# Kernel tuning notes

Measured on AMD Instinct MI355X. Metric: run time of the kernel, lower is better.

The kernel has to match this reference:

```python
import jax, jax.numpy as jnp
import numpy as np
import math

B, C, H, W = 8, 64, 256, 256
E, NH = 256, 8
HD = E // NH  # 32


def get_coords(h, w):
    xx, yy = jnp.meshgrid(jnp.arange(h, dtype=jnp.float32), jnp.arange(w, dtype=jnp.float32), indexing='ij')
    return jnp.stack((xx.reshape(-1), yy.reshape(-1)), axis=-1)  # [N, 2]


def setup_inputs() -> dict:
    key = jax.random.key(0)
    ks = jax.random.split(key, 12)
    def xavier(k, shape):
        fan_out, fan_in = shape
        a = math.sqrt(6.0 / (fan_in + fan_out))
        return jax.random.uniform(k, shape, jnp.float32, -a, a)
    x = jax.random.normal(ks[0], (B, C, H, W), jnp.float32)
    z = jax.random.normal(ks[1], (B, C), jnp.float32)
    pos = jax.random.uniform(ks[2], (B, NH, 2), jnp.float32) * (H - 1)
    Wq = xavier(ks[3], (E, C)); bq = jnp.zeros((E,), jnp.float32)
    Wk = xavier(ks[4], (E, C)); bk = jnp.zeros((E,), jnp.float32)
    Wv = xavier(ks[5], (E, C)); bv = jnp.zeros((E,), jnp.float32)
    Wp = xavier(ks[6], (HD, 2)); bp = jax.random.uniform(ks[7], (HD,), jnp.float32, -1.0, 1.0) / math.sqrt(2.0)
    return {"x": x, "z": z, "pos": pos, "Wq": Wq, "bq": bq, "Wk": Wk, "bk": bk,
            "Wv": Wv, "bv": bv, "Wp": Wp, "bp": bp}


def reference(x, z, pos, Wq, bq, Wk, bk, Wv, bv, Wp, bp):
    b, c, h, w = x.shape
    n = h * w
    x_flat = x.reshape(b, c, n).transpose(0, 2, 1)          # [B, N, C]
    pos_grid = get_coords(h, w)                              # [N, 2]
    q = (z @ Wq.T + bq).reshape(b, NH, HD)                   # [B, H, hd]
    k = (x_flat @ Wk.T + bk).reshape(b, n, NH, HD)           # [B, N, H, hd]
    # relative-position modulation of keys
    rel = pos_grid[None, :, None, :] - pos[:, None, :, :]    # [B, N, H, 2]
    qxk = rel @ Wp.T + bp                                    # [B, N, H, hd]
    k = k * qxk
    v = x_flat @ Wv.T + bv                                   # [B, N, E]
    attn_logits = jnp.einsum('bhc,bnhc->bnh', q, k) / math.sqrt(HD)
    attention = jax.nn.softmax(attn_logits, axis=1)          # softmax over N
    pos_out = jnp.einsum('bnh,nx->bhx', attention, pos_grid) # [B, H, 2]
    values = jnp.einsum('bnh,bnc->bhc', attention, v)        # [B, H, E]
    return (values, pos_out)
```

## Files before the change

### kernel.cpp

```cpp
#include <hip/hip_runtime.h>

#define NN    65536
#define NSUB  128
#define NBLK  (NN/NSUB)

typedef short bf16x8 __attribute__((ext_vector_type(8)));
typedef float f32x4v __attribute__((ext_vector_type(4)));
typedef unsigned short ushort_t;
typedef unsigned int uint_t;

#define XSTR   72
#define XHI_B  0
#define XLO_B  18432
#define LGA_B  18432
#define LGSTR  28
#define RED_B  36864
#define SMEM_BYTES 37056

#define WTHI_B  0
#define WTLO_B  32768
#define CJ_B    65536
#define PM_B    66304
#define PL_B    197376
#define PSP_B   328448
#define PSX_B   590592
#define Q_B     8979200
#define QSTR    68

__device__ __forceinline__ uint_t bf16_rne_bits(float f) {
  uint_t u = __float_as_uint(f);
  return (u + 0x7FFFu + ((u >> 16) & 1u)) >> 16;
}
template <int CTRL>
__device__ __forceinline__ float dpp_add(float x) {
  int t = __builtin_amdgcn_update_dpp(0, __float_as_int(x), CTRL, 0xf, 0xf, false);
  return x + __int_as_float(t);
}
template <int CTRL>
__device__ __forceinline__ float dpp_maxs(float x) {
  int t = __builtin_amdgcn_update_dpp((int)0xFF800000u, __float_as_int(x), CTRL, 0xf, 0xf, false);
  return fmaxf(x, __int_as_float(t));
}
__device__ __forceinline__ float wave_sum(float x) {
  x = dpp_add<0x111>(x); x = dpp_add<0x112>(x); x = dpp_add<0x114>(x);
  x = dpp_add<0x118>(x); x = dpp_add<0x142>(x); x = dpp_add<0x143>(x);
  return __int_as_float(__builtin_amdgcn_readlane(__float_as_int(x), 63));
}
__device__ __forceinline__ float wave_max(float x) {
  x = dpp_maxs<0x111>(x); x = dpp_maxs<0x112>(x); x = dpp_maxs<0x114>(x);
  x = dpp_maxs<0x118>(x); x = dpp_maxs<0x142>(x); x = dpp_maxs<0x143>(x);
  return __int_as_float(__builtin_amdgcn_readlane(__float_as_int(x), 63));
}

__global__ __launch_bounds__(64) void prep_kernel(
    const float* __restrict__ z,  const float* __restrict__ Wq, const float* __restrict__ bq,
    const float* __restrict__ Wk, const float* __restrict__ bk,
    const float* __restrict__ Wp, const float* __restrict__ bp,
    ushort_t* __restrict__ WThi, ushort_t* __restrict__ WTlo, float* __restrict__ Cj)
{
  const int h = blockIdx.x, b = blockIdx.y, t = threadIdx.x;
  __shared__ float q[32];
  if (t < 32) {
    const int e = h*32 + t;
    float a = bq[e];
    const float* zr = z + b*64;
    const float* wr = Wq + e*64;
    #pragma unroll 8
    for (int c = 0; c < 64; ++c) a += zr[c]*wr[c];
    q[t] = a;
  }
  __syncthreads();
  const int c = t;
  float w[3] = {0.f, 0.f, 0.f};
  #pragma unroll 4
  for (int hd = 0; hd < 32; ++hd) {
    const float qk = q[hd] * Wk[(h*32+hd)*64 + c];
    w[0] += qk * bp[hd];
    w[1] += qk * Wp[hd*2+0];
    w[2] += qk * Wp[hd*2+1];
  }
  #pragma unroll
  for (int j = 0; j < 3; ++j) {
    const int coeff = h*3 + j;
    const uint_t hb = bf16_rne_bits(w[j]);
    const float  fh = __uint_as_float(hb << 16);
    const uint_t lb = bf16_rne_bits(w[j] - fh);
    WThi[(b*32 + coeff)*64 + c] = (ushort_t)hb;
    WTlo[(b*32 + coeff)*64 + c] = (ushort_t)lb;
  }
  if (h == 0) {
    #pragma unroll
    for (int r = 0; r < 8; ++r) {
      WThi[(b*32 + 24 + r)*64 + c] = 0;
      WTlo[(b*32 + 24 + r)*64 + c] = 0;
    }
  }
  if (t < 3) {
    float s = 0.f;
    for (int hd = 0; hd < 32; ++hd) {
      const float m = (t == 0) ? bp[hd] : Wp[hd*2 + (t-1)];
      s += q[hd] * m * bk[h*32+hd];
    }
    Cj[b*24 + h*3 + t] = s;
  }
}

__global__ __launch_bounds__(128, 2) void main_kernel(
    const float* __restrict__ x, const float* __restrict__ pos,
    const ushort_t* __restrict__ WThi, const ushort_t* __restrict__ WTlo,
    const float* __restrict__ Cj,
    float* __restrict__ Pm, float* __restrict__ Pl,
    float* __restrict__ Psp, float* __restrict__ Psx)
{
  extern __shared__ char smc[];
  ushort_t* xhi = (ushort_t*)(smc + XHI_B);
  float*    lga = (float*)(smc + LGA_B);
  float*    red = (float*)(smc + RED_B);
  const int t   = threadIdx.x;
  const int blk = blockIdx.x;
  const int b   = blockIdx.y;
  const int n0  = blk * NSUB;
  const int wid = t >> 6, lid = t & 63;
  const int c0  = lid & 15, q4 = lid >> 4;

  bf16x8 bh[2][2], bl[2][2];
  {
    const ushort_t* wtb_h = WThi + b*2048;
    const ushort_t* wtb_l = WTlo + b*2048;
    #pragma unroll
    for (int nt = 0; nt < 2; ++nt)
      #pragma unroll
      for (int ks = 0; ks < 2; ++ks) {
        const int off = (nt*16 + c0)*64 + ks*32 + q4*8;
        bh[nt][ks] = *(const bf16x8*)(wtb_h + off);
        bl[nt][ks] = *(const bf16x8*)(wtb_l + off);
      }
  }

  {
    const float* xg = x + (size_t)b*64*NN + n0 + t;
    #pragma unroll
    for (int half = 0; half < 2; ++half) {
      float v[32];
      #pragma unroll
      for (int i = 0; i < 32; ++i) v[i] = xg[(size_t)(half*32+i)*NN];
      #pragma unroll
      for (int cc2 = 0; cc2 < 2; ++cc2) {
        const int cc = half*2 + cc2;
        uint_t hb[16], lb[16];
        #pragma unroll
        for (int i = 0; i < 16; ++i) {
          const float f = v[cc2*16+i];
          hb[i] = bf16_rne_bits(f);
          lb[i] = bf16_rne_bits(f - __uint_as_float(hb[i] << 16));
        }
        uint4 H0 = make_uint4(hb[0]|(hb[1]<<16), hb[2]|(hb[3]<<16), hb[4]|(hb[5]<<16), hb[6]|(hb[7]<<16));
        uint4 H1 = make_uint4(hb[8]|(hb[9]<<16), hb[10]|(hb[11]<<16), hb[12]|(hb[13]<<16), hb[14]|(hb[15]<<16));
        uint4 L0 = make_uint4(lb[0]|(lb[1]<<16), lb[2]|(lb[3]<<16), lb[4]|(lb[5]<<16), lb[6]|(lb[7]<<16));
        uint4 L1 = make_uint4(lb[8]|(lb[9]<<16), lb[10]|(lb[11]<<16), lb[12]|(lb[13]<<16), lb[14]|(lb[15]<<16));
        char* dh = smc + XHI_B + t*144 + cc*32;
        char* dl = smc + XLO_B + t*144 + cc*32;
        *(uint4*)(dh)      = H0;  *(uint4*)(dh + 16) = H1;
        *(uint4*)(dl)      = L0;  *(uint4*)(dl + 16) = L1;
      }
    }
  }

  float cj[24];
  {
    const float* cjp = Cj + b*24;
    #pragma unroll
    for (int k = 0; k < 24; ++k) cj[k] = cjp[k];
  }
  const int gx = blk >> 1;
  float rxh[8], py[8];
  #pragma unroll
  for (int h = 0; h < 8; ++h) {
    rxh[h] = (float)gx - pos[(b*8+h)*2 + 0];
    py[h]  = pos[(b*8+h)*2 + 1];
  }

  __syncthreads();

  f32x4v acc[4][2];
  #pragma unroll
  for (int mt = 0; mt < 4; ++mt) { acc[mt][0] = (f32x4v)0.f; acc[mt][1] = (f32x4v)0.f; }
  {
    const int mrow0 = wid*64;
    #pragma unroll
    for (int mt = 0; mt < 4; ++mt) {
      const int row = mrow0 + mt*16 + c0;
      const ushort_t* ph = xhi + row*XSTR + q4*8;
      const ushort_t* pl = (ushort_t*)(smc + XLO_B) + row*XSTR + q4*8;
      bf16x8 ah0 = *(const bf16x8*)(ph);
      bf16x8 ah1 = *(const bf16x8*)(ph + 32);
      bf16x8 al0 = *(const bf16x8*)(pl);
      bf16x8 al1 = *(const bf16x8*)(pl + 32);
      #pragma unroll
      for (int nt = 0; nt < 2; ++nt) {
        f32x4v a = acc[mt][nt];
        a = __builtin_amdgcn_mfma_f32_16x16x32_bf16(ah0, bh[nt][0], a, 0, 0, 0);
        a = __builtin_amdgcn_mfma_f32_16x16x32_bf16(ah1, bh[nt][1], a, 0, 0, 0);
        a = __builtin_amdgcn_mfma_f32_16x16x32_bf16(ah0, bl[nt][0], a, 0, 0, 0);
        a = __builtin_amdgcn_mfma_f32_16x16x32_bf16(ah1, bl[nt][1], a, 0, 0, 0);
        a = __builtin_amdgcn_mfma_f32_16x16x32_bf16(al0, bh[nt][0], a, 0, 0, 0);
        a = __builtin_amdgcn_mfma_f32_16x16x32_bf16(al1, bh[nt][1], a, 0, 0, 0);
        acc[mt][nt] = a;
      }
    }
  }
  __syncthreads();

  {
    const int mrow0 = wid*64;
    #pragma unroll
    for (int mt = 0; mt < 4; ++mt)
      #pragma unroll
      for (int r = 0; r < 4; ++r) {
        const int prow = mrow0 + mt*16 + q4*4 + r;
        lga[prow*LGSTR + c0] = acc[mt][0][r];
        if (c0 < 8) lga[prow*LGSTR + 16 + c0] = acc[mt][1][r];
      }
  }
  __syncthreads();

  float a24[24];
  {
    const float4* ap = (const float4*)(lga + t*LGSTR);
    #pragma unroll
    for (int r = 0; r < 6; ++r) *(float4*)(a24 + 4*r) = ap[r];
  }
  const float tf = (float)(((blk & 1) << 7) + t);
  float lg[8];
  #pragma unroll
  for (int h = 0; h < 8; ++h) {
    const float a0 = a24[h*3+0] + cj[h*3+0];
    const float a1 = a24[h*3+1] + cj[h*3+1];
    const float a2 = a24[h*3+2] + cj[h*3+2];
    lg[h] = (a0 + rxh[h]*a1 + (tf - py[h])*a2) * 0.17677669529663687f;
  }

  #pragma unroll
  for (int h = 0; h < 8; ++h) {
    const float m = wave_max(lg[h]);
    if (lid == 0) red[h*2 + wid] = m;
  }
  __syncthreads();

  float p[8];
  #pragma unroll
  for (int h = 0; h < 8; ++h) {
    const float M = fmaxf(red[h*2+0], red[h*2+1]);
    p[h] = __expf(lg[h] - M);
  }
  #pragma unroll
  for (int h = 0; h < 8; ++h) {
    const float sp  = wave_sum(p[h]);
    const float spj = wave_sum(p[h] * tf);
    if (lid == 0) { red[16 + h*2 + wid] = sp; red[32 + h*2 + wid] = spj; }
  }
  __syncthreads();

  if (t < 8) {
    const int base = (b*NBLK + blk)*8 + t;
    const float M  = fmaxf(red[t*2+0], red[t*2+1]);
    const float L  = red[16+t*2+0] + red[16+t*2+1];
    const float SJ = red[32+t*2+0] + red[32+t*2+1];
    Pm[base] = M;
    Pl[base] = L;
    Psp[base*2+0] = (float)gx * L;
    Psp[base*2+1] = SJ;
  }

  float aB[8];
  #pragma unroll
  for (int h = 0; h < 8; ++h) aB[h] = 0.f;
  {
    const ushort_t* xrow = xhi + (wid*64)*XSTR + lid;
    #pragma unroll 8
    for (int j = 0; j < 64; ++j) {
      const float xv = __uint_as_float(((uint_t)xrow[j*XSTR]) << 16);
      #pragma unroll
      for (int h = 0; h < 8; ++h) {
        const float pj = __int_as_float(__builtin_amdgcn_readlane(__float_as_int(p[h]), j));
        aB[h] = fmaf(pj, xv, aB[h]);
      }
    }
  }
  __syncthreads();
  {
    float* pstage = (float*)smc;
    #pragma unroll
    for (int h = 0; h < 8; ++h) pstage[(wid*8 + h)*64 + lid] = aB[h];
  }
  __syncthreads();
  {
    const float* pstage = (const float*)smc;
    const size_t pb = ((size_t)(b*NBLK + blk))*8;
    #pragma unroll
    for (int r = 0; r < 4; ++r) {
      const int idx = t + 128*r;
      const float s = pstage[idx] + pstage[512+idx];
      Psx[pb*64 + idx] = s;
    }
  }
}

__global__ __launch_bounds__(256) void reduce1_kernel(
    const float* __restrict__ Pm, const float* __restrict__ Pl,
    const float* __restrict__ Psp, const float* __restrict__ Psx,
    float* __restrict__ Q)
{
  const int g = blockIdx.x, h = blockIdx.y, b = blockIdx.z, t = threadIdx.x;
  __shared__ float al[64];
  __shared__ float mgs;
  __shared__ float sums[3];
  __shared__ float sxl[256];
  const int base = (b*NBLK + g*64)*8 + h;

  float m_t = -1e30f;
  if (t < 64) {
    m_t = Pm[base + t*8];
    float mm = m_t;
    #pragma unroll
    for (int off = 32; off >= 1; off >>= 1) mm = fmaxf(mm, __shfl_xor(mm, off, 64));
    if (t == 0) mgs = mm;
  }
  __syncthreads();
  const float Mg = mgs;
  if (t < 64) {
    const float a = __expf(m_t - Mg);
    al[t] = a;
    float lt = Pl[base + t*8] * a;
    float sx = Psp[(base + t*8)*2 + 0] * a;
    float sy = Psp[(base + t*8)*2 + 1] * a;
    #pragma unroll
    for (int off = 32; off >= 1; off >>= 1) {
      lt += __shfl_xor(lt, off, 64);
      sx += __shfl_xor(sx, off, 64);
      sy += __shfl_xor(sy, off, 64);
    }
    if (t == 0) { sums[0] = lt; sums[1] = sx; sums[2] = sy; }
  }
  __syncthreads();
  {
    const int c = t & 63, g2 = t >> 6;
    float acc = 0.f;
    #pragma unroll
    for (int i = 0; i < 16; ++i) {
      const int k = g2*16 + i;
      acc += al[k] * Psx[(size_t)(base + k*8)*64 + c];
    }
    sxl[g2*64 + c] = acc;
  }
  __syncthreads();
  float* q = Q + ((b*8 + h)*8 + g)*QSTR;
  if (t < 64) q[4+t] = sxl[t] + sxl[64+t] + sxl[128+t] + sxl[192+t];
  if (t == 0) { q[0] = Mg; q[1] = sums[0]; q[2] = sums[1]; q[3] = sums[2]; }
}

__global__ __launch_bounds__(64) void reduce2_kernel(
    const float* __restrict__ Q, const float* __restrict__ Wv, const float* __restrict__ bv,
    float* __restrict__ out)
{
  const int h = blockIdx.x, b = blockIdx.y, t = threadIdx.x;
  __shared__ float qm[8], bl[8], l8[8], sx8[8], sy8[8];
  __shared__ float SXs[64];
  const float* qb = Q + ((b*8 + h)*8)*QSTR;

  if (t < 8) qm[t] = qb[t*QSTR + 0];
  __syncthreads();
  float M = qm[0];
  #pragma unroll
  for (int g = 1; g < 8; ++g) M = fmaxf(M, qm[g]);
  if (t < 8) {
    const float be = __expf(qm[t] - M);
    bl[t]  = be;
    l8[t]  = be * qb[t*QSTR + 1];
    sx8[t] = be * qb[t*QSTR + 2];
    sy8[t] = be * qb[t*QSTR + 3];
  }
  __syncthreads();
  float L = 0.f;
  #pragma unroll
  for (int g = 0; g < 8; ++g) L += l8[g];
  const float invL = 1.0f / L;
  {
    float s = 0.f;
    #pragma unroll
    for (int g = 0; g < 8; ++g) s += bl[g] * qb[g*QSTR + 4 + t];
    SXs[t] = s * invL;
  }
  __syncthreads();

  #pragma unroll
  for (int r = 0; r < 4; ++r) {
    const int e = t + 64*r;
    float v = bv[e];
    const float* wvr = Wv + e*64;
    #pragma unroll 8
    for (int c = 0; c < 64; ++c) v += wvr[c] * SXs[c];
    out[(b*8 + h)*256 + e] = v;
  }
  if (t == 0) {
    float spx = 0.f, spy = 0.f;
    #pragma unroll
    for (int g = 0; g < 8; ++g) { spx += sx8[g]; spy += sy8[g]; }
    out[16384 + (b*8 + h)*2 + 0] = spx * invL;
    out[16384 + (b*8 + h)*2 + 1] = spy * invL;
  }
}

extern "C" void kernel_launch(void* const* d_in, const int* in_sizes, int n_in,
                              void* d_out, int out_size, void* d_ws, size_t ws_size,
                              hipStream_t stream)
{
  const float* x   = (const float*)d_in[0];
  const float* z   = (const float*)d_in[1];
  const float* pos = (const float*)d_in[2];
  const float* Wq  = (const float*)d_in[3];
  const float* bq  = (const float*)d_in[4];
  const float* Wk  = (const float*)d_in[5];
  const float* bk  = (const float*)d_in[6];
  const float* Wv  = (const float*)d_in[7];
  const float* bv  = (const float*)d_in[8];
  const float* Wp  = (const float*)d_in[9];
  const float* bp  = (const float*)d_in[10];
  float* out = (float*)d_out;
  char*  wsb = (char*)d_ws;

  ushort_t* WThi = (ushort_t*)(wsb + WTHI_B);
  ushort_t* WTlo = (ushort_t*)(wsb + WTLO_B);
  float* Cj  = (float*)(wsb + CJ_B);
  float* Pm  = (float*)(wsb + PM_B);
  float* Pl  = (float*)(wsb + PL_B);
  float* Psp = (float*)(wsb + PSP_B);
  float* Psx = (float*)(wsb + PSX_B);
  float* Q   = (float*)(wsb + Q_B);

  prep_kernel   <<<dim3(8,8),    64,  0,          stream>>>(z, Wq, bq, Wk, bk, Wp, bp, WThi, WTlo, Cj);
  main_kernel   <<<dim3(NBLK,8), 128, SMEM_BYTES, stream>>>(x, pos, WThi, WTlo, Cj, Pm, Pl, Psp, Psx);
  reduce1_kernel<<<dim3(8,8,8),  256, 0,          stream>>>(Pm, Pl, Psp, Psx, Q);
  reduce2_kernel<<<dim3(8,8),    64,  0,          stream>>>(Q, Wv, bv, out);
}
```

Measured before the change: 253.8 us.

## Compute attention-weighted x partial sums with MFMA on split bf16 probabilities

Replaces the per-lane readlane/FMA loop that accumulates p·x for each head with bf16 MFMA instructions. The probabilities are split into hi/lo bf16 parts, staged in LDS and used as the A operand, which removes the LDS staging reduction and one barrier. The x global loads are also issued all at once (64 values per thread), and the lo bf16 part is now truncated instead of rounded. These changes trade some register pressure and precision (x uses only its hi part in this product, lo-part truncation) for less scalar ALU work.

Result: faster. 237.7 us (-6.3%).

```diff
diff --git a/kernel.cpp b/kernel.cpp
--- a/kernel.cpp
+++ b/kernel.cpp
@@ -14,6 +14,7 @@
 #define XLO_B  18432
 #define LGA_B  18432
 #define LGSTR  28
+#define PSTR   136
 #define RED_B  36864
 #define SMEM_BYTES 37056
 
@@ -139,30 +140,26 @@
 
   {
     const float* xg = x + (size_t)b*64*NN + n0 + t;
-    #pragma unroll
-    for (int half = 0; half < 2; ++half) {
-      float v[32];
+    float v[64];
+    #pragma unroll
+    for (int i = 0; i < 64; ++i) v[i] = xg[(size_t)i*NN];
+    #pragma unroll
+    for (int cc = 0; cc < 4; ++cc) {
+      uint_t hb[16], lb[16];
       #pragma unroll
-      for (int i = 0; i < 32; ++i) v[i] = xg[(size_t)(half*32+i)*NN];
-      #pragma unroll
-      for (int cc2 = 0; cc2 < 2; ++cc2) {
-        const int cc = half*2 + cc2;
-        uint_t hb[16], lb[16];
-        #pragma unroll
-        for (int i = 0; i < 16; ++i) {
-          const float f = v[cc2*16+i];
-          hb[i] = bf16_rne_bits(f);
-          lb[i] = bf16_rne_bits(f - __uint_as_float(hb[i] << 16));
-        }
-        uint4 H0 = make_uint4(hb[0]|(hb[1]<<16), hb[2]|(hb[3]<<16), hb[4]|(hb[5]<<16), hb[6]|(hb[7]<<16));
-        uint4 H1 = make_uint4(hb[8]|(hb[9]<<16), hb[10]|(hb[11]<<16), hb[12]|(hb[13]<<16), hb[14]|(hb[15]<<16));
-        uint4 L0 = make_uint4(lb[0]|(lb[1]<<16), lb[2]|(lb[3]<<16), lb[4]|(lb[5]<<16), lb[6]|(lb[7]<<16));
-        uint4 L1 = make_uint4(lb[8]|(lb[9]<<16), lb[10]|(lb[11]<<16), lb[12]|(lb[13]<<16), lb[14]|(lb[15]<<16));
-        char* dh = smc + XHI_B + t*144 + cc*32;
-        char* dl = smc + XLO_B + t*144 + cc*32;
-        *(uint4*)(dh)      = H0;  *(uint4*)(dh + 16) = H1;
-        *(uint4*)(dl)      = L0;  *(uint4*)(dl + 16) = L1;
-      }
+      for (int i = 0; i < 16; ++i) {
+        const float f = v[cc*16+i];
+        hb[i] = bf16_rne_bits(f);
+        lb[i] = __float_as_uint(f - __uint_as_float(hb[i] << 16)) >> 16;
+      }
+      uint4 H0 = make_uint4(hb[0]|(hb[1]<<16), hb[2]|(hb[3]<<16), hb[4]|(hb[5]<<16), hb[6]|(hb[7]<<16));
+      uint4 H1 = make_uint4(hb[8]|(hb[9]<<16), hb[10]|(hb[11]<<16), hb[12]|(hb[13]<<16), hb[14]|(hb[15]<<16));
+      uint4 L0 = make_uint4(lb[0]|(lb[1]<<16), lb[2]|(lb[3]<<16), lb[4]|(lb[5]<<16), lb[6]|(lb[7]<<16));
+      uint4 L1 = make_uint4(lb[8]|(lb[9]<<16), lb[10]|(lb[11]<<16), lb[12]|(lb[13]<<16), lb[14]|(lb[15]<<16));
+      char* dh = smc + XHI_B + t*144 + cc*32;
+      char* dl = smc + XLO_B + t*144 + cc*32;
+      *(uint4*)(dh)      = H0;  *(uint4*)(dh + 16) = H1;
+      *(uint4*)(dl)      = L0;  *(uint4*)(dl + 16) = L1;
     }
   }
 
@@ -253,6 +250,19 @@
     const float M = fmaxf(red[h*2+0], red[h*2+1]);
     p[h] = __expf(lg[h] - M);
   }
+
+  {
+    ushort_t* pls = (ushort_t*)(smc + LGA_B);
+    #pragma unroll
+    for (int h = 0; h < 8; ++h) {
+      const uint_t hb = bf16_rne_bits(p[h]);
+      const float  hf = __uint_as_float(hb << 16);
+      const uint_t lb = __float_as_uint(p[h] - hf) >> 16;
+      pls[h*PSTR + t]       = (ushort_t)hb;
+      pls[(h+8)*PSTR + t]   = (ushort_t)lb;
+    }
+  }
+
   #pragma unroll
   for (int h = 0; h < 8; ++h) {
     const float sp  = wave_sum(p[h]);
@@ -272,36 +282,39 @@
     Psp[base*2+1] = SJ;
   }
 
-  float aB[8];
-  #pragma unroll
-  for (int h = 0; h < 8; ++h) aB[h] = 0.f;
-  {
-    const ushort_t* xrow = xhi + (wid*64)*XSTR + lid;
-    #pragma unroll 8
-    for (int j = 0; j < 64; ++j) {
-      const float xv = __uint_as_float(((uint_t)xrow[j*XSTR]) << 16);
+  {
+    const ushort_t* pls = (const ushort_t*)(smc + LGA_B);
+    bf16x8 afr[4];
+    #pragma unroll
+    for (int ks = 0; ks < 4; ++ks)
+      afr[ks] = *(const bf16x8*)(pls + c0*PSTR + ks*32 + q4*8);
+
+    f32x4v accB0 = (f32x4v)0.f, accB1 = (f32x4v)0.f;
+    const int chbase = wid*32 + c0;
+    #pragma unroll
+    for (int ks = 0; ks < 4; ++ks) {
+      const ushort_t* xcol = xhi + (ks*32 + q4*8)*XSTR + chbase;
+      bf16x8 b0, b1;
       #pragma unroll
-      for (int h = 0; h < 8; ++h) {
-        const float pj = __int_as_float(__builtin_amdgcn_readlane(__float_as_int(p[h]), j));
-        aB[h] = fmaf(pj, xv, aB[h]);
-      }
-    }
-  }
-  __syncthreads();
-  {
-    float* pstage = (float*)smc;
-    #pragma unroll
-    for (int h = 0; h < 8; ++h) pstage[(wid*8 + h)*64 + lid] = aB[h];
-  }
-  __syncthreads();
-  {
-    const float* pstage = (const float*)smc;
-    const size_t pb = ((size_t)(b*NBLK + blk))*8;
+      for (int i = 0; i < 8; ++i) {
+        b0[i] = (short)xcol[i*XSTR];
+        b1[i] = (short)xcol[i*XSTR + 16];
+      }
+      accB0 = __builtin_amdgcn_mfma_f32_16x16x32_bf16(afr[ks], b0, accB0, 0, 0, 0);
+      accB1 = __builtin_amdgcn_mfma_f32_16x16x32_bf16(afr[ks], b1, accB1, 0, 0, 0);
+    }
+
+    const size_t pb64 = ((size_t)(b*NBLK + blk))*8*64;
     #pragma unroll
     for (int r = 0; r < 4; ++r) {
-      const int idx = t + 128*r;
-      const float s = pstage[idx] + pstage[512+idx];
-      Psx[pb*64 + idx] = s;
+      const float o0 = __shfl_xor(accB0[r], 32, 64);
+      const float o1 = __shfl_xor(accB1[r], 32, 64);
+      if (q4 < 2) {
+        const int h = q4*4 + r;
+        const int c = wid*32 + c0;
+        Psx[pb64 + h*64 + c]      = accB0[r] + o0;
+        Psx[pb64 + h*64 + c + 16] = accB1[r] + o1;
+      }
     }
   }
 }
```
